# Optimization experiments

Hardware: AMD Instinct MI355X
Metric: run time of the kernel (lower is better)

## Reference

```python
import jax, jax.numpy as jnp
import numpy as np
from jax import lax

G = 8  # number of RBF grid points (FastKAN default style)
GRID = jnp.linspace(-2.0, 2.0, G)
DENOM = 4.0 / (G - 1)  # grid spacing used as gaussian width


def _fastkan_conv(x, ln_w, ln_b, Wb, bb, Ws):
    # x: [B, C, H, W]; 3x3 conv, stride 1, pad 1 via patch unfold + FastKAN linear
    B, C, H, W = x.shape
    p = lax.conv_general_dilated_patches(x, (3, 3), (1, 1), ((1, 1), (1, 1)))  # [B, C*9, H, W]
    p = p.transpose(0, 2, 3, 1).reshape(B * H * W, C * 9)  # [N, in]
    # LayerNorm over patch features (FastKAN normalizes before the RBF basis)
    mu = p.mean(-1, keepdims=True)
    var = p.var(-1, keepdims=True)
    pn = (p - mu) / jnp.sqrt(var + 1e-5) * ln_w + ln_b
    # Gaussian RBF basis: [N, in, G]
    rbf = jnp.exp(-jnp.square((pn[:, :, None] - GRID) / DENOM))
    spline = rbf.reshape(B * H * W, -1) @ Ws.T          # [N, out]
    base = jax.nn.silu(p) @ Wb.T + bb                    # [N, out]
    out = spline + base
    return out.reshape(B, H, W, -1).transpose(0, 3, 1, 2)  # [B, out, H, W]


def _bn_relu_pool(h, gamma, beta):
    # BatchNorm2d in training mode (batch stats), ReLU, MaxPool2d(2,2)
    mu = h.mean((0, 2, 3), keepdims=True)
    var = h.var((0, 2, 3), keepdims=True)
    h = (h - mu) / jnp.sqrt(var + 1e-5) * gamma[None, :, None, None] + beta[None, :, None, None]
    h = jax.nn.relu(h)
    return lax.reduce_window(h, -jnp.inf, lax.max, (1, 1, 2, 2), (1, 1, 2, 2), 'VALID')


def setup_inputs() -> dict:
    key = jax.random.key(0)
    ks = jax.random.split(key, 16)
    B, Cin, H, W = 32, 16, 64, 64
    dims = [(Cin * 9, 64), (64 * 9, 128), (128 * 9, 256)]
    inp = {"x": jax.random.normal(ks[0], (B, Cin, H, W), jnp.float32)}
    for i, (fin, fout) in enumerate(dims, 1):
        inp[f"ln_w{i}"] = jnp.ones((fin,), jnp.float32)
        inp[f"ln_b{i}"] = jnp.zeros((fin,), jnp.float32)
        inp[f"Wb{i}"] = jax.random.normal(ks[3 * i], (fout, fin), jnp.float32) * 0.05
        inp[f"bb{i}"] = jnp.zeros((fout,), jnp.float32)
        inp[f"Ws{i}"] = jax.random.normal(ks[3 * i + 1], (fout, fin * G), jnp.float32) * 0.05
        inp[f"g{i}"] = jnp.ones((fout,), jnp.float32)
        inp[f"be{i}"] = jnp.zeros((fout,), jnp.float32)
    return inp


def reference(x, ln_w1, ln_b1, Wb1, bb1, Ws1, g1, be1,
              ln_w2, ln_b2, Wb2, bb2, Ws2, g2, be2,
              ln_w3, ln_b3, Wb3, bb3, Ws3, g3, be3):
    h = _bn_relu_pool(_fastkan_conv(x, ln_w1, ln_b1, Wb1, bb1, Ws1), g1, be1)
    h = _bn_relu_pool(_fastkan_conv(h, ln_w2, ln_b2, Wb2, bb2, Ws2), g2, be2)
    h = _bn_relu_pool(_fastkan_conv(h, ln_w3, ln_b3, Wb3, bb3, Ws3), g3, be3)
    return h.reshape(h.shape[0], -1)  # flatten: [B, 256*8*8]
```

## Files before the change

### kernel.cpp

```cpp
#include <hip/hip_runtime.h>

typedef _Float16 half_t;
typedef __attribute__((ext_vector_type(8))) _Float16 half8;
typedef __attribute__((ext_vector_type(4))) float floatx4;


#define RBF_SCALE 2.1019644f

template<int C, int H, int W>
__global__ __launch_bounds__(256)
void ln_prep(const float* __restrict__ x,
             const float* __restrict__ lnw, const float* __restrict__ lnb,
             half_t* __restrict__ pn, half_t* __restrict__ sp)
{
    const int HW = H * W, IN = C * 9;
    const int NL = (IN + 63) / 64;
    const int wv = threadIdx.x >> 6, lane = threadIdx.x & 63;
    const int pix = blockIdx.x * 4 + wv;
    const int b = pix / HW, hw = pix % HW, h = hw / W, w = hw % W;
    const float* xb = x + (long)b * C * HW;

    float v[NL];
    float s = 0.f, s2 = 0.f;
    #pragma unroll
    for (int t = 0; t < NL; ++t) {
        int i = t * 64 + lane;
        float val = 0.f;
        if (i < IN) {
            int ch = i / 9, r = i - ch * 9;
            int y = h + r / 3 - 1, xx = w + r % 3 - 1;
            if (y >= 0 && y < H && xx >= 0 && xx < W)
                val = xb[ch * HW + y * W + xx];
        }
        v[t] = val; s += val; s2 += val * val;
    }
    #pragma unroll
    for (int off = 32; off > 0; off >>= 1) {
        s  += __shfl_down(s,  off, 64);
        s2 += __shfl_down(s2, off, 64);
    }
    s = __shfl(s, 0, 64); s2 = __shfl(s2, 0, 64);
    float mean = s / IN;
    float istd = rsqrtf(s2 / IN - mean * mean + 1e-5f);

    #pragma unroll
    for (int t = 0; t < NL; ++t) {
        int i = t * 64 + lane;
        if (i < IN) {
            float val = v[t];
            float pnv = (val - mean) * istd * lnw[i] + lnb[i];
            pn[(long)pix * IN + i] = (half_t)(pnv * RBF_SCALE);
            sp[(long)pix * IN + i] = (half_t)(val / (1.f + __expf(-val)));
        }
    }
}

template<int IN, int OUT, int KPAD>
__global__ __launch_bounds__(256)
void conv_w(const float* __restrict__ Ws, const float* __restrict__ Wb,
            half_t* __restrict__ Wt)
{
    int idx = blockIdx.x * 256 + threadIdx.x;
    if (idx >= OUT * KPAD) return;
    int s = idx & 63;
    int t = idx >> 6;
    int o = t % OUT;
    int it = t / OUT;
    int k = it * 64 + (((s >> 3) ^ (o & 7)) << 3) + (s & 7);
    float v = 0.f;
    if (k < IN * 9) {
        int j = k / IN, i = k - j * IN;
        v = (j < 8) ? Ws[(long)o * IN * 8 + i * 8 + j] : Wb[(long)o * IN + i];
    }
    Wt[idx] = (half_t)v;
}

template<int IN, int OUT, int HW, int NB, int SPLIT>
__global__ __launch_bounds__(256)
void kan_gemm(const half_t* __restrict__ pn, const half_t* __restrict__ sp,
              const half_t* __restrict__ Wt, float* __restrict__ out)
{
    const int K = IN * 9, KPAD = (K + 63) & ~63, KIT = KPAD / 64;

    __shared__ half_t As[64 * 64];
    __shared__ half_t Bs[NB * 64 * 64];

    const int tid = threadIdx.x;
    const int row = tid >> 2, q = tid & 3;
    const int pix = blockIdx.x * 64 + row;
    const half_t* pnrow = pn + (long)pix * IN;
    const half_t* sprow = sp + (long)pix * IN;

    const int wv = tid >> 6, lane = tid & 63;
    const int lr = lane & 15, lq = lane >> 4;
    const int u0 = (2 * q) ^ (row & 7);
    const int u1 = (2 * q + 1) ^ (row & 7);

    floatx4 acc[NB][4] = {};

    const int it0 = (blockIdx.z * KIT) / SPLIT;
    const int it1 = ((blockIdx.z + 1) * KIT) / SPLIT;

    for (int it = it0; it < it1; ++it) {
        const int k0 = it * 64;
        __syncthreads();

        {
            const half_t* ws = Wt + (long)it * OUT * 64 + wv * (NB * 2 * 512);
            #pragma unroll
            for (int c = 0; c < NB * 2; ++c) {
                __builtin_amdgcn_global_load_lds(
                    (const __attribute__((address_space(1))) void*)(ws + c * 512 + lane * 8),
                    (__attribute__((address_space(3))) void*)(&Bs[wv * (NB * 2 * 512) + c * 512]),
                    16, 0, 0);
            }
        }

        {
            int cs = k0 + q * 16;
            int j = cs / IN;
            half8 a0, a1;
            if (j < 8) {
                int i0 = cs - j * IN;
                float gj = RBF_SCALE * (-2.f + j * (4.f / 7.f));
                half8 p0 = *(const half8*)(pnrow + i0);
                half8 p1 = *(const half8*)(pnrow + i0 + 8);
                #pragma unroll
                for (int kk = 0; kk < 8; ++kk) {
                    float v0 = (float)p0[kk] - gj;
                    a0[kk] = (half_t)__builtin_amdgcn_exp2f(-(v0 * v0));
                    float v1 = (float)p1[kk] - gj;
                    a1[kk] = (half_t)__builtin_amdgcn_exp2f(-(v1 * v1));
                }
            } else if (j == 8) {
                int i0 = cs - 8 * IN;
                a0 = *(const half8*)(sprow + i0);
                a1 = *(const half8*)(sprow + i0 + 8);
            } else {
                a0 = half8{}; a1 = half8{};
            }
            *(half8*)&As[row * 64 + u0 * 8] = a0;
            *(half8*)&As[row * 64 + u1 * 8] = a1;
        }
        __syncthreads();

        #pragma unroll
        for (int ks = 0; ks < 2; ++ks) {
            half8 af[4], bf[NB];
            #pragma unroll
            for (int mf = 0; mf < 4; ++mf) {
                int r = mf * 16 + lr;
                af[mf] = *(const half8*)&As[r * 64 + (((ks * 4 + lq) ^ (r & 7)) * 8)];
            }
            #pragma unroll
            for (int nb = 0; nb < NB; ++nb) {
                int r = wv * NB * 16 + nb * 16 + lr;
                bf[nb] = *(const half8*)&Bs[r * 64 + (((ks * 4 + lq) ^ (r & 7)) * 8)];
            }
            #pragma unroll
            for (int nb = 0; nb < NB; ++nb)
                #pragma unroll
                for (int mf = 0; mf < 4; ++mf)
                    acc[nb][mf] = __builtin_amdgcn_mfma_f32_16x16x32_f16(
                        bf[nb], af[mf], acc[nb][mf], 0, 0, 0);
        }
    }

    const long zoff = (long)blockIdx.z * ((long)gridDim.x * 64) * OUT;
    #pragma unroll
    for (int nb = 0; nb < NB; ++nb)
    #pragma unroll
    for (int mf = 0; mf < 4; ++mf)
    #pragma unroll
    for (int reg = 0; reg < 4; ++reg) {
        int o  = wv * NB * 16 + nb * 16 + lq * 4 + reg;
        int p2 = blockIdx.x * 64 + mf * 16 + lr;
        int b2 = p2 / HW, hw2 = p2 % HW;
        out[zoff + ((long)b2 * OUT + o) * HW + hw2] = acc[nb][mf][reg];
    }
}

__launch_bounds__(256)
__global__ void bn_stats(const float* __restrict__ h, const float* __restrict__ bias,
                         int C, int HW, int B, int nz, float* __restrict__ sums)
{
    int c = blockIdx.y;
    float bbc = bias[c];
    long zstride = (long)B * C * HW;
    int total = B * HW;
    float s = 0.f, s2 = 0.f;
    for (int idx = blockIdx.x * 256 + threadIdx.x; idx < total; idx += 256 * gridDim.x) {
        int b = idx / HW, r = idx % HW;
        long base = ((long)b * C + c) * HW + r;
        float v = bbc;
        for (int z = 0; z < nz; ++z) v += h[z * zstride + base];
        s += v; s2 += v * v;
    }
    for (int off = 32; off > 0; off >>= 1) {
        s  += __shfl_down(s,  off, 64);
        s2 += __shfl_down(s2, off, 64);
    }
    __shared__ float rs[4], rs2[4];
    int lane = threadIdx.x & 63, wid = threadIdx.x >> 6;
    if (lane == 0) { rs[wid] = s; rs2[wid] = s2; }
    __syncthreads();
    if (threadIdx.x == 0) {
        atomicAdd(&sums[c],     rs[0] + rs[1] + rs[2] + rs[3]);
        atomicAdd(&sums[C + c], rs2[0] + rs2[1] + rs2[2] + rs2[3]);
    }
}

__launch_bounds__(256)
__global__ void bn_relu_pool(const float* __restrict__ h, const float* __restrict__ sums,
                             const float* __restrict__ bias,
                             const float* __restrict__ gamma, const float* __restrict__ beta,
                             float* __restrict__ out, int B, int C, int H, int W, int nz)
{
    int Ho = H / 2, Wo = W / 2;
    long total = (long)B * C * Ho * Wo;
    long idx = (long)blockIdx.x * 256 + threadIdx.x;
    if (idx >= total) return;
    int pw = idx % Wo; long t = idx / Wo;
    int ph = t % Ho; t /= Ho;
    int c = t % C; int b = (int)(t / C);

    float M = (float)B * H * W;
    float mean = sums[c] / M;
    float var  = sums[C + c] / M - mean * mean;
    float scale = gamma[c] * rsqrtf(var + 1e-5f);
    float shift = beta[c] - mean * scale + bias[c] * scale;

    long zstride = (long)B * C * H * W;
    const float* hp = h + ((long)b * C + c) * H * W;
    float m = 0.f;
    #pragma unroll
    for (int i = 0; i < 2; ++i)
        #pragma unroll
        for (int j = 0; j < 2; ++j) {
            long off = (2 * ph + i) * W + 2 * pw + j;
            float v = 0.f;
            for (int z = 0; z < nz; ++z) v += hp[z * zstride + off];
            v = v * scale + shift;
            m = fmaxf(m, v);
        }
    out[idx] = m;
}

extern "C" void kernel_launch(void* const* d_in, const int* in_sizes, int n_in,
                              void* d_out, int out_size, void* d_ws, size_t ws_size,
                              hipStream_t stream) {
    const float* x     = (const float*)d_in[0];
    const float* ln_w1 = (const float*)d_in[1];  const float* ln_b1 = (const float*)d_in[2];
    const float* Wb1   = (const float*)d_in[3];  const float* bb1   = (const float*)d_in[4];
    const float* Ws1   = (const float*)d_in[5];  const float* g1    = (const float*)d_in[6];
    const float* be1   = (const float*)d_in[7];
    const float* ln_w2 = (const float*)d_in[8];  const float* ln_b2 = (const float*)d_in[9];
    const float* Wb2   = (const float*)d_in[10]; const float* bb2   = (const float*)d_in[11];
    const float* Ws2   = (const float*)d_in[12]; const float* g2    = (const float*)d_in[13];
    const float* be2   = (const float*)d_in[14];
    const float* ln_w3 = (const float*)d_in[15]; const float* ln_b3 = (const float*)d_in[16];
    const float* Wb3   = (const float*)d_in[17]; const float* bb3   = (const float*)d_in[18];
    const float* Ws3   = (const float*)d_in[19]; const float* g3    = (const float*)d_in[20];
    const float* be3   = (const float*)d_in[21];

    const int B = 32;
    char* ws = (char*)d_ws;
    float*  convbuf = (float*)(ws + 0);
    float*  poolbuf = (float*)(ws + 33554432);
    float*  stats1  = (float*)(ws + 41943040);
    float*  stats2  = (float*)(ws + 41945088);
    float*  stats3  = (float*)(ws + 41947136);
    half_t* wt1     = (half_t*)(ws + 41949184);
    half_t* wt2     = (half_t*)(ws + 42121216);
    half_t* wt3     = (half_t*)(ws + 43448320);
    half_t* pnbuf   = (half_t*)(ws + 48756736);
    half_t* spbuf   = (half_t*)(ws + 86505472);

    hipMemsetAsync(stats1, 0, 6144, stream);

    conv_w<144, 64, 1344><<<(64 * 1344 + 255) / 256, 256, 0, stream>>>(Ws1, Wb1, wt1);
    conv_w<576, 128, 5184><<<(128 * 5184 + 255) / 256, 256, 0, stream>>>(Ws2, Wb2, wt2);
    conv_w<1152, 256, 10368><<<(256 * 10368 + 255) / 256, 256, 0, stream>>>(Ws3, Wb3, wt3);

    {
        const int H = 64, W = 64, OUT = 64;
        int npix = B * H * W;
        ln_prep<16, H, W><<<npix / 4, 256, 0, stream>>>(x, ln_w1, ln_b1, pnbuf, spbuf);
        kan_gemm<144, OUT, H * W, 1, 1><<<dim3(npix / 64, 1, 1), 256, 0, stream>>>(
            pnbuf, spbuf, wt1, convbuf);
        bn_stats<<<dim3(64, OUT), 256, 0, stream>>>(convbuf, bb1, OUT, H * W, B, 1, stats1);
        long tot = (long)B * OUT * (H / 2) * (W / 2);
        bn_relu_pool<<<(tot + 255) / 256, 256, 0, stream>>>(
            convbuf, stats1, bb1, g1, be1, poolbuf, B, OUT, H, W, 1);
    }
    {
        const int H = 32, W = 32, OUT = 128;
        int npix = B * H * W;
        ln_prep<64, H, W><<<npix / 4, 256, 0, stream>>>(poolbuf, ln_w2, ln_b2, pnbuf, spbuf);
        kan_gemm<576, OUT, H * W, 2, 2><<<dim3(npix / 64, 1, 2), 256, 0, stream>>>(
            pnbuf, spbuf, wt2, convbuf);
        bn_stats<<<dim3(16, OUT), 256, 0, stream>>>(convbuf, bb2, OUT, H * W, B, 2, stats2);
        long tot = (long)B * OUT * (H / 2) * (W / 2);
        bn_relu_pool<<<(tot + 255) / 256, 256, 0, stream>>>(
            convbuf, stats2, bb2, g2, be2, poolbuf, B, OUT, H, W, 2);
    }
    {
        const int H = 16, W = 16, OUT = 256;
        int npix = B * H * W;
        ln_prep<128, H, W><<<npix / 4, 256, 0, stream>>>(poolbuf, ln_w3, ln_b3, pnbuf, spbuf);
        kan_gemm<1152, OUT, H * W, 4, 4><<<dim3(npix / 64, 1, 4), 256, 0, stream>>>(
            pnbuf, spbuf, wt3, convbuf);
        bn_stats<<<dim3(8, OUT), 256, 0, stream>>>(convbuf, bb3, OUT, H * W, B, 4, stats3);
        long tot = (long)B * OUT * (H / 2) * (W / 2);
        bn_relu_pool<<<(tot + 255) / 256, 256, 0, stream>>>(
            convbuf, stats3, bb3, g3, be3, (float*)d_out, B, OUT, H, W, 4);
    }
}
```

Measured before the change: 485.1 us.

## Double-buffer A tile and load B weights directly into registers

The KAN GEMM now keeps the weight (B) fragments in registers, loaded straight from global memory in the MFMA fragment layout, instead of staging them through LDS with global_load_lds. The A tile (RBF/SiLU activations) is double-buffered in LDS, and the next iteration's global loads are issued before the current MFMAs, leaving one barrier per iteration. The weight pre-layout drops its XOR swizzle to match the new access pattern. This trades more VGPRs (two sets of B fragments plus prefetched A) for overlap of memory latency with compute, which may reduce occupancy. Each wave now fetches B separately from global memory/cache rather than through shared LDS.

```diff
diff --git a/kernel.cpp b/kernel.cpp
--- a/kernel.cpp
+++ b/kernel.cpp
@@ -66,7 +66,7 @@
     int t = idx >> 6;
     int o = t % OUT;
     int it = t / OUT;
-    int k = it * 64 + (((s >> 3) ^ (o & 7)) << 3) + (s & 7);
+    int k = it * 64 + s;
     float v = 0.f;
     if (k < IN * 9) {
         int j = k / IN, i = k - j * IN;
@@ -82,8 +82,7 @@
 {
     const int K = IN * 9, KPAD = (K + 63) & ~63, KIT = KPAD / 64;
 
-    __shared__ half_t As[64 * 64];
-    __shared__ half_t Bs[NB * 64 * 64];
+    __shared__ half_t As[2][64 * 64];
 
     const int tid = threadIdx.x;
     const int row = tid >> 2, q = tid & 3;
@@ -101,69 +100,84 @@
     const int it0 = (blockIdx.z * KIT) / SPLIT;
     const int it1 = ((blockIdx.z + 1) * KIT) / SPLIT;
 
-    for (int it = it0; it < it1; ++it) {
-        const int k0 = it * 64;
-        __syncthreads();
-
-        {
-            const half_t* ws = Wt + (long)it * OUT * 64 + wv * (NB * 2 * 512);
+    half8 ra0_0, ra0_1, ra1_0, ra1_1;
+    int ja0, ja1;
+    half8 b0[NB][2], b1[NB][2];
+
+    auto loadA = [&](int it, half8& r0, half8& r1, int& j) {
+        int cs = it * 64 + q * 16;
+        j = cs / IN;
+        const half_t* src = pnrow;
+        if (j < 8)       src = pnrow + (cs - j * IN);
+        else if (j == 8) src = sprow + (cs - 8 * IN);
+        r0 = *(const half8*)src;
+        r1 = *(const half8*)(src + 8);
+    };
+    auto loadB = [&](int it, half8 (&b)[NB][2]) {
+        const half_t* base = Wt + ((long)it * OUT + wv * NB * 16 + lr) * 64 + lq * 8;
+        #pragma unroll
+        for (int nb = 0; nb < NB; ++nb)
             #pragma unroll
-            for (int c = 0; c < NB * 2; ++c) {
-                __builtin_amdgcn_global_load_lds(
-                    (const __attribute__((address_space(1))) void*)(ws + c * 512 + lane * 8),
-                    (__attribute__((address_space(3))) void*)(&Bs[wv * (NB * 2 * 512) + c * 512]),
-                    16, 0, 0);
+            for (int ks = 0; ks < 2; ++ks)
+                b[nb][ks] = *(const half8*)(base + nb * 16 * 64 + ks * 32);
+    };
+    auto writeA = [&](int buf, half8 r0, half8 r1, int j) {
+        half8 a0, a1;
+        if (j < 8) {
+            float gj = RBF_SCALE * (-2.f + j * (4.f / 7.f));
+            #pragma unroll
+            for (int kk = 0; kk < 8; ++kk) {
+                float v0 = (float)r0[kk] - gj;
+                a0[kk] = (half_t)__builtin_amdgcn_exp2f(-(v0 * v0));
+                float v1 = (float)r1[kk] - gj;
+                a1[kk] = (half_t)__builtin_amdgcn_exp2f(-(v1 * v1));
             }
-        }
-
-        {
-            int cs = k0 + q * 16;
-            int j = cs / IN;
-            half8 a0, a1;
-            if (j < 8) {
-                int i0 = cs - j * IN;
-                float gj = RBF_SCALE * (-2.f + j * (4.f / 7.f));
-                half8 p0 = *(const half8*)(pnrow + i0);
-                half8 p1 = *(const half8*)(pnrow + i0 + 8);
-                #pragma unroll
-                for (int kk = 0; kk < 8; ++kk) {
-                    float v0 = (float)p0[kk] - gj;
-                    a0[kk] = (half_t)__builtin_amdgcn_exp2f(-(v0 * v0));
-                    float v1 = (float)p1[kk] - gj;
-                    a1[kk] = (half_t)__builtin_amdgcn_exp2f(-(v1 * v1));
-                }
-            } else if (j == 8) {
-                int i0 = cs - 8 * IN;
-                a0 = *(const half8*)(sprow + i0);
-                a1 = *(const half8*)(sprow + i0 + 8);
-            } else {
-                a0 = half8{}; a1 = half8{};
-            }
-            *(half8*)&As[row * 64 + u0 * 8] = a0;
-            *(half8*)&As[row * 64 + u1 * 8] = a1;
-        }
-        __syncthreads();
-
+        } else if (j == 8) {
+            a0 = r0; a1 = r1;
+        } else {
+            a0 = half8{}; a1 = half8{};
+        }
+        *(half8*)&As[buf][row * 64 + u0 * 8] = a0;
+        *(half8*)&As[buf][row * 64 + u1 * 8] = a1;
+    };
+    auto domfma = [&](int buf, half8 (&b)[NB][2]) {
+        __builtin_amdgcn_s_setprio(1);
         #pragma unroll
         for (int ks = 0; ks < 2; ++ks) {
-            half8 af[4], bf[NB];
+            half8 af[4];
             #pragma unroll
             for (int mf = 0; mf < 4; ++mf) {
                 int r = mf * 16 + lr;
-                af[mf] = *(const half8*)&As[r * 64 + (((ks * 4 + lq) ^ (r & 7)) * 8)];
-            }
-            #pragma unroll
-            for (int nb = 0; nb < NB; ++nb) {
-                int r = wv * NB * 16 + nb * 16 + lr;
-                bf[nb] = *(const half8*)&Bs[r * 64 + (((ks * 4 + lq) ^ (r & 7)) * 8)];
+                af[mf] = *(const half8*)&As[buf][r * 64 + (((ks * 4 + lq) ^ (r & 7)) * 8)];
             }
             #pragma unroll
             for (int nb = 0; nb < NB; ++nb)
                 #pragma unroll
                 for (int mf = 0; mf < 4; ++mf)
                     acc[nb][mf] = __builtin_amdgcn_mfma_f32_16x16x32_f16(
-                        bf[nb], af[mf], acc[nb][mf], 0, 0, 0);
-        }
+                        b[nb][ks], af[mf], acc[nb][mf], 0, 0, 0);
+        }
+        __builtin_amdgcn_s_setprio(0);
+    };
+
+    loadA(it0, ra0_0, ra0_1, ja0);
+    loadB(it0, b0);
+    writeA(0, ra0_0, ra0_1, ja0);
+    __syncthreads();
+
+    for (int it = it0; it < it1; it += 2) {
+        bool m1 = (it + 1 < it1);
+        if (m1) { loadA(it + 1, ra1_0, ra1_1, ja1); loadB(it + 1, b1); }
+        domfma(0, b0);
+        if (m1) writeA(1, ra1_0, ra1_1, ja1);
+        __syncthreads();
+        if (!m1) break;
+
+        bool m2 = (it + 2 < it1);
+        if (m2) { loadA(it + 2, ra0_0, ra0_1, ja0); loadB(it + 2, b0); }
+        domfma(1, b1);
+        if (m2) writeA(0, ra0_0, ra0_1, ja0);
+        __syncthreads();
     }
 
     const long zoff = (long)blockIdx.z * ((long)gridDim.x * 64) * OUT;
```

New measurement: 578.6 us. 19.3% more time.

## Reorder K loop by input block and compute gaussian RBFs by recurrence

Applied to the files above, without the earlier changes.

The weight layout now orders K as input-block-major with the 9 basis terms (8 RBF plus SiLU) inner, and the GEMM loop walks that order. Each thread loads pn once per input block and produces the 8 Gaussians with a multiplicative recurrence: two exp2 calls, then a multiply per grid point, instead of one exp2 per grid point. This cuts transcendental work and repeated pn loads in the A-tile builder. In exchange it adds clamping of pn (to keep the recurrence from overflowing in fp32), extra padding for layer 1 (144 inputs padded to 192), a larger workspace and s_setprio hints around the MFMA section.

```diff
diff --git a/kernel.cpp b/kernel.cpp
--- a/kernel.cpp
+++ b/kernel.cpp
@@ -6,6 +6,10 @@
 
 
 #define RBF_SCALE 2.1019644f
+#define RBF_G0   -4.2039288f
+#define RBF_2D    2.40224482f
+#define RBF_D2    1.44269504f
+#define RBF_Q     0.13533528f
 
 template<int C, int H, int W>
 __global__ __launch_bounds__(256)
@@ -49,29 +53,31 @@
         if (i < IN) {
             float val = v[t];
             float pnv = (val - mean) * istd * lnw[i] + lnb[i];
-            pn[(long)pix * IN + i] = (half_t)(pnv * RBF_SCALE);
+            pnv = fminf(12.f, fmaxf(-12.f, pnv * RBF_SCALE));
+            pn[(long)pix * IN + i] = (half_t)pnv;
             sp[(long)pix * IN + i] = (half_t)(val / (1.f + __expf(-val)));
         }
     }
 }
 
-template<int IN, int OUT, int KPAD>
+template<int IN, int OUT>
 __global__ __launch_bounds__(256)
 void conv_w(const float* __restrict__ Ws, const float* __restrict__ Wb,
             half_t* __restrict__ Wt)
 {
+    const int NIB = (IN + 63) / 64, NSTEP = NIB * 9;
     int idx = blockIdx.x * 256 + threadIdx.x;
-    if (idx >= OUT * KPAD) return;
-    int s = idx & 63;
+    if (idx >= OUT * NSTEP * 64) return;
+    int uu = idx & 63;
     int t = idx >> 6;
     int o = t % OUT;
-    int it = t / OUT;
-    int k = it * 64 + (((s >> 3) ^ (o & 7)) << 3) + (s & 7);
+    int s = t / OUT;
+    int iblk = s / 9, j = s % 9;
+    int ulin = (((uu >> 3) ^ (o & 7)) << 3) + (uu & 7);
+    int i = iblk * 64 + ulin;
     float v = 0.f;
-    if (k < IN * 9) {
-        int j = k / IN, i = k - j * IN;
+    if (i < IN)
         v = (j < 8) ? Ws[(long)o * IN * 8 + i * 8 + j] : Wb[(long)o * IN + i];
-    }
     Wt[idx] = (half_t)v;
 }
 
@@ -80,7 +86,7 @@
 void kan_gemm(const half_t* __restrict__ pn, const half_t* __restrict__ sp,
               const half_t* __restrict__ Wt, float* __restrict__ out)
 {
-    const int K = IN * 9, KPAD = (K + 63) & ~63, KIT = KPAD / 64;
+    const int NIB = (IN + 63) / 64;
 
     __shared__ half_t As[64 * 64];
     __shared__ half_t Bs[NB * 64 * 64];
@@ -97,12 +103,13 @@
     const int u1 = (2 * q + 1) ^ (row & 7);
 
     floatx4 acc[NB][4] = {};
-
-    const int it0 = (blockIdx.z * KIT) / SPLIT;
-    const int it1 = ((blockIdx.z + 1) * KIT) / SPLIT;
-
-    for (int it = it0; it < it1; ++it) {
-        const int k0 = it * 64;
+    float r[16], u[16];
+
+    const int grpA = (blockIdx.z * NIB) / SPLIT;
+    const int grpB = ((blockIdx.z + 1) * NIB) / SPLIT;
+
+    int j = 0, iblk = grpA;
+    for (int it = grpA * 9; it < grpB * 9; ++it) {
         __syncthreads();
 
         {
@@ -117,45 +124,60 @@
         }
 
         {
-            int cs = k0 + q * 16;
-            int j = cs / IN;
-            half8 a0, a1;
+            const int i0 = iblk * 64 + q * 16;
+            const bool ok = (i0 < IN);
             if (j < 8) {
-                int i0 = cs - j * IN;
-                float gj = RBF_SCALE * (-2.f + j * (4.f / 7.f));
-                half8 p0 = *(const half8*)(pnrow + i0);
-                half8 p1 = *(const half8*)(pnrow + i0 + 8);
+                if (j == 0) {
+                    const half_t* pp = pnrow + (ok ? i0 : 0);
+                    half8 p0 = *(const half8*)pp;
+                    half8 p1 = *(const half8*)(pp + 8);
+                    #pragma unroll
+                    for (int kk = 0; kk < 8; ++kk) {
+                        float t0 = (float)p0[kk], t1 = (float)p1[kk];
+                        float d0 = t0 - RBF_G0, d1 = t1 - RBF_G0;
+                        r[kk]     = ok ? __builtin_amdgcn_exp2f(-(d0 * d0)) : 0.f;
+                        u[kk]     = ok ? __builtin_amdgcn_exp2f(fmaf(RBF_2D, d0, -RBF_D2)) : 0.f;
+                        r[kk + 8] = ok ? __builtin_amdgcn_exp2f(-(d1 * d1)) : 0.f;
+                        u[kk + 8] = ok ? __builtin_amdgcn_exp2f(fmaf(RBF_2D, d1, -RBF_D2)) : 0.f;
+                    }
+                }
+                half8 a0, a1;
                 #pragma unroll
                 for (int kk = 0; kk < 8; ++kk) {
-                    float v0 = (float)p0[kk] - gj;
-                    a0[kk] = (half_t)__builtin_amdgcn_exp2f(-(v0 * v0));
-                    float v1 = (float)p1[kk] - gj;
-                    a1[kk] = (half_t)__builtin_amdgcn_exp2f(-(v1 * v1));
+                    a0[kk] = (half_t)r[kk];
+                    a1[kk] = (half_t)r[kk + 8];
                 }
-            } else if (j == 8) {
-                int i0 = cs - 8 * IN;
-                a0 = *(const half8*)(sprow + i0);
-                a1 = *(const half8*)(sprow + i0 + 8);
+                *(half8*)&As[row * 64 + u0 * 8] = a0;
+                *(half8*)&As[row * 64 + u1 * 8] = a1;
+                if (j < 7) {
+                    #pragma unroll
+                    for (int kk = 0; kk < 16; ++kk) { r[kk] *= u[kk]; u[kk] *= RBF_Q; }
+                }
             } else {
-                a0 = half8{}; a1 = half8{};
+                half8 a0 = half8{}, a1 = half8{};
+                if (ok) {
+                    a0 = *(const half8*)(sprow + i0);
+                    a1 = *(const half8*)(sprow + i0 + 8);
+                }
+                *(half8*)&As[row * 64 + u0 * 8] = a0;
+                *(half8*)&As[row * 64 + u1 * 8] = a1;
             }
-            *(half8*)&As[row * 64 + u0 * 8] = a0;
-            *(half8*)&As[row * 64 + u1 * 8] = a1;
         }
         __syncthreads();
 
+        __builtin_amdgcn_s_setprio(1);
         #pragma unroll
         for (int ks = 0; ks < 2; ++ks) {
             half8 af[4], bf[NB];
             #pragma unroll
             for (int mf = 0; mf < 4; ++mf) {
-                int r = mf * 16 + lr;
-                af[mf] = *(const half8*)&As[r * 64 + (((ks * 4 + lq) ^ (r & 7)) * 8)];
+                int rr = mf * 16 + lr;
+                af[mf] = *(const half8*)&As[rr * 64 + (((ks * 4 + lq) ^ (rr & 7)) * 8)];
             }
             #pragma unroll
             for (int nb = 0; nb < NB; ++nb) {
-                int r = wv * NB * 16 + nb * 16 + lr;
-                bf[nb] = *(const half8*)&Bs[r * 64 + (((ks * 4 + lq) ^ (r & 7)) * 8)];
+                int rr = wv * NB * 16 + nb * 16 + lr;
+                bf[nb] = *(const half8*)&Bs[rr * 64 + (((ks * 4 + lq) ^ (rr & 7)) * 8)];
             }
             #pragma unroll
             for (int nb = 0; nb < NB; ++nb)
@@ -164,6 +186,9 @@
                     acc[nb][mf] = __builtin_amdgcn_mfma_f32_16x16x32_f16(
                         bf[nb], af[mf], acc[nb][mf], 0, 0, 0);
         }
+        __builtin_amdgcn_s_setprio(0);
+
+        if (++j == 9) { j = 0; ++iblk; }
     }
 
     const long zoff = (long)blockIdx.z * ((long)gridDim.x * 64) * OUT;
@@ -271,16 +296,16 @@
     float*  stats2  = (float*)(ws + 41945088);
     float*  stats3  = (float*)(ws + 41947136);
     half_t* wt1     = (half_t*)(ws + 41949184);
-    half_t* wt2     = (half_t*)(ws + 42121216);
-    half_t* wt3     = (half_t*)(ws + 43448320);
-    half_t* pnbuf   = (half_t*)(ws + 48756736);
-    half_t* spbuf   = (half_t*)(ws + 86505472);
+    half_t* wt2     = (half_t*)(ws + 42170368);
+    half_t* wt3     = (half_t*)(ws + 43497472);
+    half_t* pnbuf   = (half_t*)(ws + 48805888);
+    half_t* spbuf   = (half_t*)(ws + 86554624);
 
     hipMemsetAsync(stats1, 0, 6144, stream);
 
-    conv_w<144, 64, 1344><<<(64 * 1344 + 255) / 256, 256, 0, stream>>>(Ws1, Wb1, wt1);
-    conv_w<576, 128, 5184><<<(128 * 5184 + 255) / 256, 256, 0, stream>>>(Ws2, Wb2, wt2);
-    conv_w<1152, 256, 10368><<<(256 * 10368 + 255) / 256, 256, 0, stream>>>(Ws3, Wb3, wt3);
+    conv_w<144, 64><<<(64 * 27 * 64 + 255) / 256, 256, 0, stream>>>(Ws1, Wb1, wt1);
+    conv_w<576, 128><<<(128 * 81 * 64 + 255) / 256, 256, 0, stream>>>(Ws2, Wb2, wt2);
+    conv_w<1152, 256><<<(256 * 162 * 64 + 255) / 256, 256, 0, stream>>>(Ws3, Wb3, wt3);
 
     {
         const int H = 64, W = 64, OUT = 64;
```

Measured after the change: 493.1 us. No clear change (+1.6%).
